# Optimization experiments

Hardware: AMD Instinct MI355X
Metric: run time of the kernel (lower is better)

The kernel has to match this reference:

```python
import jax, jax.numpy as jnp
import numpy as np

BATCH, SEQ, IN, HID, OUT = 4096, 512, 2, 128, 1


def setup_inputs() -> dict:
    key = jax.random.key(0)
    k_x, k_wih, k_bih, k_who, k_bho = jax.random.split(key, 5)
    s = 1.0 / np.sqrt(IN + HID)
    return {
        "x": jax.random.normal(k_x, (BATCH, SEQ, IN), dtype=jnp.float32),
        "W_ih": jax.random.normal(k_wih, (HID, IN + HID), dtype=jnp.float32) * s,
        "b_ih": jax.random.normal(k_bih, (HID,), dtype=jnp.float32) * s,
        "W_ho": jax.random.normal(k_who, (OUT, HID), dtype=jnp.float32) / np.sqrt(HID),
        "b_bho" if False else "b_ho": jax.random.normal(k_bho, (OUT,), dtype=jnp.float32) / np.sqrt(HID),
    }


def reference(x, W_ih, b_ih, W_ho, b_ho):
    # x: [B, T, I]. Elman cell: h = tanh([x_t, h] @ W_ih^T + b_ih)
    B = x.shape[0]
    h0 = jnp.zeros((B, W_ih.shape[0]), dtype=x.dtype)
    # split W_ih into input and hidden blocks (equivalent to concat+matmul)
    W_x = W_ih[:, : x.shape[-1]]   # [H, I]
    W_h = W_ih[:, x.shape[-1] :]   # [H, H]

    def step(h, x_t):
        h_new = jnp.tanh(x_t @ W_x.T + h @ W_h.T + b_ih)
        return h_new, None

    xs = jnp.swapaxes(x, 0, 1)  # [T, B, I] for scan over time
    h_final, _ = jax.lax.scan(step, h0, xs)
    return h_final @ W_ho.T + b_ho  # [B, OUT]
```

## Files before the change

kernel.cpp:

```cpp
#include <hip/hip_runtime.h>


constexpr int BATCH   = 4096;
constexpr int SEQ     = 512;
constexpr int INP     = 2;
constexpr int HID     = 128;
constexpr int BM      = 16;
constexpr int THREADS = 512;
constexpr int XCHUNK  = 128;

typedef short bf16x8 __attribute__((ext_vector_type(8)));
typedef float f32x4  __attribute__((ext_vector_type(4)));

__device__ inline unsigned short f2bf(float f) {
    unsigned u = __float_as_uint(f);
    return (unsigned short)((u + 0x7FFFu + ((u >> 16) & 1u)) >> 16);
}
__device__ inline float bf2f(unsigned short s) {
    return __uint_as_float(((unsigned)s) << 16);
}

__global__ __launch_bounds__(THREADS, 2)
void elman_mfma6(const float* __restrict__ x,
                 const float* __restrict__ W_ih,
                 const float* __restrict__ b_ih,
                 const float* __restrict__ W_ho,
                 const float* __restrict__ b_ho,
                 float* __restrict__ out)
{
    __shared__ unsigned short hlds[2][2][BM][HID];
    __shared__ float xs[BM][XCHUNK][INP];
    __shared__ float red[BM][8];

    const int tid  = threadIdx.x;
    const int lane = tid & 63;
    const int w    = tid >> 6;
    const int l15  = lane & 15;
    const int g    = lane >> 4;
    const int j    = w * 16 + l15;
    const int B0   = blockIdx.x * BM;

    bf16x8 bhi[4], blo[4];
    {
        const float* Wrow = W_ih + (size_t)j * (INP + HID) + INP;
        #pragma unroll
        for (int kt = 0; kt < 4; ++kt) {
            const int k0 = kt * 32 + g * 8;
            #pragma unroll
            for (int i = 0; i < 8; ++i) {
                const float wv = Wrow[k0 + i];
                const unsigned short hi = f2bf(wv);
                const float lo = wv - bf2f(hi);
                bhi[kt][i] = (short)hi;
                blo[kt][i] = (short)f2bf(lo);
            }
        }
    }
    const float* Wrow0 = W_ih + (size_t)j * (INP + HID);
    const float wx0 = Wrow0[0];
    const float wx1 = Wrow0[1];
    const float bj  = b_ih[j];

    reinterpret_cast<float4*>(hlds)[tid] = float4{0.f, 0.f, 0.f, 0.f};

    {
        const int row = tid >> 5;
        const int o8  = (tid & 31) * 8;
        const float* src = x + (size_t)(B0 + row) * (SEQ * INP) + o8;
        float* dst = &xs[row][0][0] + o8;
        *reinterpret_cast<float4*>(dst)     = *reinterpret_cast<const float4*>(src);
        *reinterpret_cast<float4*>(dst + 4) = *reinterpret_cast<const float4*>(src + 4);
    }
    __syncthreads();

    int p = 0;
    float hv[4] = {0.f, 0.f, 0.f, 0.f};
    const int sw_r = l15 << 4;

    #pragma unroll 1
    for (int t = 0; t < SEQ; ++t) {
        const int tt = t & (XCHUNK - 1);
        if (t && tt == 0) {
            const int row = tid >> 5;
            const int o8  = (tid & 31) * 8;
            const float* src = x + (size_t)(B0 + row) * (SEQ * INP)
                                 + (size_t)(t >> 7) * (XCHUNK * INP) + o8;
            float* dst = &xs[row][0][0] + o8;
            *reinterpret_cast<float4*>(dst)     = *reinterpret_cast<const float4*>(src);
            *reinterpret_cast<float4*>(dst + 4) = *reinterpret_cast<const float4*>(src + 4);
            __syncthreads();
        }

        const char* hp = (const char*)&hlds[p][0][0][0];
        const char* lp = (const char*)&hlds[p][1][0][0];
        bf16x8 ahi[4], alo[4];
        #pragma unroll
        for (int kt = 0; kt < 4; ++kt) {
            const int off = l15 * 256 + ((kt * 64 + g * 16) ^ sw_r);
            ahi[kt] = *reinterpret_cast<const bf16x8*>(hp + off);
            alo[kt] = *reinterpret_cast<const bf16x8*>(lp + off);
        }

        f32x4 a0 = {0.f, 0.f, 0.f, 0.f};
        f32x4 a1 = {0.f, 0.f, 0.f, 0.f};
        f32x4 a2 = {0.f, 0.f, 0.f, 0.f};
        #pragma unroll
        for (int kt = 0; kt < 4; ++kt) {
            a0 = __builtin_amdgcn_mfma_f32_16x16x32_bf16(ahi[kt], bhi[kt], a0, 0, 0, 0);
            a1 = __builtin_amdgcn_mfma_f32_16x16x32_bf16(alo[kt], bhi[kt], a1, 0, 0, 0);
            a2 = __builtin_amdgcn_mfma_f32_16x16x32_bf16(ahi[kt], blo[kt], a2, 0, 0, 0);
        }

        unsigned short* hn = &hlds[p ^ 1][0][0][0];
        unsigned short* ln = &hlds[p ^ 1][1][0][0];
        #pragma unroll
        for (int i = 0; i < 4; ++i) {
            const int rr = g * 4 + i;
            const float2 xv = *reinterpret_cast<const float2*>(&xs[rr][tt][0]);
            const float acc = (a0[i] + a1[i] + a2[i])
                            + fmaf(wx0, xv.x, fmaf(wx1, xv.y, bj));
            const float e = __expf(2.0f * acc);
            const float h = 1.0f - __fdividef(2.0f, e + 1.0f);
            hv[i] = h;
            const unsigned short hb = f2bf(h);
            const float lo = h - bf2f(hb);
            const int off = rr * 256 + ((2 * j) ^ (rr << 4));
            *(unsigned short*)((char*)hn + off) = hb;
            *(unsigned short*)((char*)ln + off) = f2bf(lo);
        }
        __syncthreads();
        p ^= 1;
    }

    const float who = W_ho[j];
    float pr[4];
    #pragma unroll
    for (int i = 0; i < 4; ++i) {
        float v = who * hv[i];
        v += __shfl_xor(v, 1);
        v += __shfl_xor(v, 2);
        v += __shfl_xor(v, 4);
        v += __shfl_xor(v, 8);
        pr[i] = v;
    }
    if (l15 == 0) {
        #pragma unroll
        for (int i = 0; i < 4; ++i) red[g * 4 + i][w] = pr[i];
    }
    __syncthreads();
    if (tid < BM) {
        float s = b_ho[0];
        #pragma unroll
        for (int q = 0; q < 8; ++q) s += red[tid][q];
        out[B0 + tid] = s;
    }
}

extern "C" void kernel_launch(void* const* d_in, const int* in_sizes, int n_in,
                              void* d_out, int out_size, void* d_ws, size_t ws_size,
                              hipStream_t stream)
{
    (void)in_sizes; (void)n_in; (void)out_size; (void)d_ws; (void)ws_size;
    const float* x    = (const float*)d_in[0];
    const float* W_ih = (const float*)d_in[1];
    const float* b_ih = (const float*)d_in[2];
    const float* W_ho = (const float*)d_in[3];
    const float* b_ho = (const float*)d_in[4];
    float* out = (float*)d_out;

    dim3 grid(BATCH / BM);
    dim3 block(THREADS);
    elman_mfma6<<<grid, block, 0, stream>>>(x, W_ih, b_ih, W_ho, b_ho, out);
}
```

Measured before the change: 353.8 us.

## Swap MFMA operands so each lane writes four contiguous hidden values packed

The MFMA operand order is swapped so weights are the A operand and hidden state the B operand. Each lane's four accumulator outputs then correspond to four consecutive hidden units of one batch row, so the bf16 hi/lo split uses packed v_cvt_pk_bf16_f32 conversions and a single 8-byte LDS store per buffer, replacing eight scalar 2-byte stores. The x staging buffer is transposed to [t][row] so each lane reads one float2 per step instead of four, and per-unit weights, bias and W_ho are preloaded into registers. This is meant to cut LDS store and conversion instructions on the serial per-step critical path. In exchange it uses more registers and relies on the hardware round-to-nearest-even conversion matching the old manual rounding.

```diff
diff --git a/kernel.cpp b/kernel.cpp
--- a/kernel.cpp
+++ b/kernel.cpp
@@ -19,9 +19,14 @@
 __device__ inline float bf2f(unsigned short s) {
     return __uint_as_float(((unsigned)s) << 16);
 }
+__device__ inline unsigned cvt_pk_bf16(float a, float b) {
+    unsigned r;
+    asm("v_cvt_pk_bf16_f32 %0, %1, %2" : "=v"(r) : "v"(a), "v"(b));
+    return r;
+}
 
 __global__ __launch_bounds__(THREADS, 2)
-void elman_mfma6(const float* __restrict__ x,
+void elman_mfma7(const float* __restrict__ x,
                  const float* __restrict__ W_ih,
                  const float* __restrict__ b_ih,
                  const float* __restrict__ W_ho,
@@ -29,7 +34,7 @@
                  float* __restrict__ out)
 {
     __shared__ unsigned short hlds[2][2][BM][HID];
-    __shared__ float xs[BM][XCHUNK][INP];
+    __shared__ float2 xs[XCHUNK][BM];
     __shared__ float red[BM][8];
 
     const int tid  = threadIdx.x;
@@ -37,12 +42,11 @@
     const int w    = tid >> 6;
     const int l15  = lane & 15;
     const int g    = lane >> 4;
-    const int j    = w * 16 + l15;
     const int B0   = blockIdx.x * BM;
 
-    bf16x8 bhi[4], blo[4];
+    bf16x8 whi[4], wlo[4];
     {
-        const float* Wrow = W_ih + (size_t)j * (INP + HID) + INP;
+        const float* Wrow = W_ih + (size_t)(w * 16 + l15) * (INP + HID) + INP;
         #pragma unroll
         for (int kt = 0; kt < 4; ++kt) {
             const int k0 = kt * 32 + g * 8;
@@ -50,44 +54,62 @@
             for (int i = 0; i < 8; ++i) {
                 const float wv = Wrow[k0 + i];
                 const unsigned short hi = f2bf(wv);
-                const float lo = wv - bf2f(hi);
-                bhi[kt][i] = (short)hi;
-                blo[kt][i] = (short)f2bf(lo);
+                whi[kt][i] = (short)hi;
+                wlo[kt][i] = (short)f2bf(wv - bf2f(hi));
             }
         }
     }
-    const float* Wrow0 = W_ih + (size_t)j * (INP + HID);
-    const float wx0 = Wrow0[0];
-    const float wx1 = Wrow0[1];
-    const float bj  = b_ih[j];
 
-    reinterpret_cast<float4*>(hlds)[tid] = float4{0.f, 0.f, 0.f, 0.f};
+    float wx0v[4], wx1v[4], bjv[4], whov[4];
+    #pragma unroll
+    for (int reg = 0; reg < 4; ++reg) {
+        const int jj = w * 16 + g * 4 + reg;
+        const float* Wr = W_ih + (size_t)jj * (INP + HID);
+        wx0v[reg] = Wr[0];
+        wx1v[reg] = Wr[1];
+        bjv[reg]  = b_ih[jj];
+        whov[reg] = W_ho[jj];
+    }
 
+    int roff[4];
+    #pragma unroll
+    for (int kt = 0; kt < 4; ++kt)
+        roff[kt] = l15 * 256 + ((kt * 64 + g * 16) ^ (l15 << 4));
+    const int woff = l15 * 256 + (((w * 32 + (g & 2) * 8)) ^ (l15 << 4)) + (g & 1) * 8;
+
+    reinterpret_cast<float4*>(hlds)[tid]       = float4{0.f, 0.f, 0.f, 0.f};
+    reinterpret_cast<float4*>(hlds)[tid + 512] = float4{0.f, 0.f, 0.f, 0.f};
+
+    const int sr = tid >> 5;
+    const int so = (tid & 31) * 8;
     {
-        const int row = tid >> 5;
-        const int o8  = (tid & 31) * 8;
-        const float* src = x + (size_t)(B0 + row) * (SEQ * INP) + o8;
-        float* dst = &xs[row][0][0] + o8;
-        *reinterpret_cast<float4*>(dst)     = *reinterpret_cast<const float4*>(src);
-        *reinterpret_cast<float4*>(dst + 4) = *reinterpret_cast<const float4*>(src + 4);
+        const float* src = x + (size_t)(B0 + sr) * (SEQ * INP) + so;
+        const float4 v0 = *reinterpret_cast<const float4*>(src);
+        const float4 v1 = *reinterpret_cast<const float4*>(src + 4);
+        const int t0 = so >> 1;
+        xs[t0 + 0][sr] = float2{v0.x, v0.y};
+        xs[t0 + 1][sr] = float2{v0.z, v0.w};
+        xs[t0 + 2][sr] = float2{v1.x, v1.y};
+        xs[t0 + 3][sr] = float2{v1.z, v1.w};
     }
     __syncthreads();
 
     int p = 0;
     float hv[4] = {0.f, 0.f, 0.f, 0.f};
-    const int sw_r = l15 << 4;
 
     #pragma unroll 1
     for (int t = 0; t < SEQ; ++t) {
         const int tt = t & (XCHUNK - 1);
         if (t && tt == 0) {
-            const int row = tid >> 5;
-            const int o8  = (tid & 31) * 8;
-            const float* src = x + (size_t)(B0 + row) * (SEQ * INP)
-                                 + (size_t)(t >> 7) * (XCHUNK * INP) + o8;
-            float* dst = &xs[row][0][0] + o8;
-            *reinterpret_cast<float4*>(dst)     = *reinterpret_cast<const float4*>(src);
-            *reinterpret_cast<float4*>(dst + 4) = *reinterpret_cast<const float4*>(src + 4);
+            const float* src = x + (size_t)(B0 + sr) * (SEQ * INP)
+                                 + (size_t)(t >> 7) * (XCHUNK * INP) + so;
+            const float4 v0 = *reinterpret_cast<const float4*>(src);
+            const float4 v1 = *reinterpret_cast<const float4*>(src + 4);
+            const int t0 = so >> 1;
+            xs[t0 + 0][sr] = float2{v0.x, v0.y};
+            xs[t0 + 1][sr] = float2{v0.z, v0.w};
+            xs[t0 + 2][sr] = float2{v1.x, v1.y};
+            xs[t0 + 3][sr] = float2{v1.z, v1.w};
             __syncthreads();
         }
 
@@ -96,9 +118,8 @@
         bf16x8 ahi[4], alo[4];
         #pragma unroll
         for (int kt = 0; kt < 4; ++kt) {
-            const int off = l15 * 256 + ((kt * 64 + g * 16) ^ sw_r);
-            ahi[kt] = *reinterpret_cast<const bf16x8*>(hp + off);
-            alo[kt] = *reinterpret_cast<const bf16x8*>(lp + off);
+            ahi[kt] = *reinterpret_cast<const bf16x8*>(hp + roff[kt]);
+            alo[kt] = *reinterpret_cast<const bf16x8*>(lp + roff[kt]);
         }
 
         f32x4 a0 = {0.f, 0.f, 0.f, 0.f};
@@ -106,47 +127,45 @@
         f32x4 a2 = {0.f, 0.f, 0.f, 0.f};
         #pragma unroll
         for (int kt = 0; kt < 4; ++kt) {
-            a0 = __builtin_amdgcn_mfma_f32_16x16x32_bf16(ahi[kt], bhi[kt], a0, 0, 0, 0);
-            a1 = __builtin_amdgcn_mfma_f32_16x16x32_bf16(alo[kt], bhi[kt], a1, 0, 0, 0);
-            a2 = __builtin_amdgcn_mfma_f32_16x16x32_bf16(ahi[kt], blo[kt], a2, 0, 0, 0);
+            a0 = __builtin_amdgcn_mfma_f32_16x16x32_bf16(whi[kt], ahi[kt], a0, 0, 0, 0);
+            a1 = __builtin_amdgcn_mfma_f32_16x16x32_bf16(whi[kt], alo[kt], a1, 0, 0, 0);
+            a2 = __builtin_amdgcn_mfma_f32_16x16x32_bf16(wlo[kt], ahi[kt], a2, 0, 0, 0);
         }
 
-        unsigned short* hn = &hlds[p ^ 1][0][0][0];
-        unsigned short* ln = &hlds[p ^ 1][1][0][0];
+        const float2 xv = xs[tt][l15];
+        float hcur[4];
         #pragma unroll
-        for (int i = 0; i < 4; ++i) {
-            const int rr = g * 4 + i;
-            const float2 xv = *reinterpret_cast<const float2*>(&xs[rr][tt][0]);
-            const float acc = (a0[i] + a1[i] + a2[i])
-                            + fmaf(wx0, xv.x, fmaf(wx1, xv.y, bj));
-            const float e = __expf(2.0f * acc);
-            const float h = 1.0f - __fdividef(2.0f, e + 1.0f);
-            hv[i] = h;
-            const unsigned short hb = f2bf(h);
-            const float lo = h - bf2f(hb);
-            const int off = rr * 256 + ((2 * j) ^ (rr << 4));
-            *(unsigned short*)((char*)hn + off) = hb;
-            *(unsigned short*)((char*)ln + off) = f2bf(lo);
+        for (int reg = 0; reg < 4; ++reg) {
+            const float acc = (a0[reg] + a1[reg] + a2[reg])
+                            + fmaf(wx0v[reg], xv.x, fmaf(wx1v[reg], xv.y, bjv[reg]));
+            const float e = __expf(acc + acc);
+            hcur[reg] = 1.0f - __fdividef(2.0f, e + 1.0f);
+            hv[reg] = hcur[reg];
         }
+        const unsigned c01 = cvt_pk_bf16(hcur[0], hcur[1]);
+        const unsigned c23 = cvt_pk_bf16(hcur[2], hcur[3]);
+        const float h0b = __uint_as_float(c01 << 16);
+        const float h1b = __uint_as_float(c01 & 0xFFFF0000u);
+        const float h2b = __uint_as_float(c23 << 16);
+        const float h3b = __uint_as_float(c23 & 0xFFFF0000u);
+        const unsigned l01 = cvt_pk_bf16(hcur[0] - h0b, hcur[1] - h1b);
+        const unsigned l23 = cvt_pk_bf16(hcur[2] - h2b, hcur[3] - h3b);
+
+        char* hn = (char*)&hlds[p ^ 1][0][0][0];
+        char* ln = (char*)&hlds[p ^ 1][1][0][0];
+        *reinterpret_cast<uint2*>(hn + woff) = uint2{c01, c23};
+        *reinterpret_cast<uint2*>(ln + woff) = uint2{l01, l23};
+
         __syncthreads();
         p ^= 1;
     }
 
-    const float who = W_ho[j];
-    float pr[4];
+    float part = 0.f;
     #pragma unroll
-    for (int i = 0; i < 4; ++i) {
-        float v = who * hv[i];
-        v += __shfl_xor(v, 1);
-        v += __shfl_xor(v, 2);
-        v += __shfl_xor(v, 4);
-        v += __shfl_xor(v, 8);
-        pr[i] = v;
-    }
-    if (l15 == 0) {
-        #pragma unroll
-        for (int i = 0; i < 4; ++i) red[g * 4 + i][w] = pr[i];
-    }
+    for (int reg = 0; reg < 4; ++reg) part = fmaf(whov[reg], hv[reg], part);
+    part += __shfl_xor(part, 16);
+    part += __shfl_xor(part, 32);
+    if (lane < 16) red[l15][w] = part;
     __syncthreads();
     if (tid < BM) {
         float s = b_ho[0];
@@ -170,5 +189,5 @@
 
     dim3 grid(BATCH / BM);
     dim3 block(THREADS);
-    elman_mfma6<<<grid, block, 0, stream>>>(x, W_ih, b_ih, W_ho, b_ho, out);
+    elman_mfma7<<<grid, block, 0, stream>>>(x, W_ih, b_ih, W_ho, b_ho, out);
 }
```

After: 329.0 us. 7.0% less time.
